# Performance work log

Hardware: AMD Instinct MI355X
Metric: run time of the kernel (lower is better)

Reference implementation:

```python
import jax, jax.numpy as jnp
import numpy as np

D = 256      # d_model
NH = 8       # num_heads
NP = 4       # n_points
H = 100      # feature map height (single level)
W = 100      # feature map width
B = 4
Q = H * W
S = H * W


def setup_inputs() -> dict:
    key = jax.random.key(0)
    ks = jax.random.split(key, 12)
    p = lambda k, shp, s=0.02: jax.random.normal(k, shp, jnp.float32) * s
    return {
        "hidden_states": jax.random.normal(ks[0], (B, Q, D), jnp.float32),
        "encoder_hidden_states": jax.random.normal(ks[1], (B, S, D), jnp.float32),
        "reference_points": jax.random.uniform(ks[2], (B, Q, 1, 2), jnp.float32),
        "spatial_shapes": jnp.array([[H, W]], dtype=jnp.int32),
        "W_off": p(ks[3], (NH * NP * 2, D)),
        "b_off": p(ks[4], (NH * NP * 2,), 0.5),
        "W_attn": p(ks[5], (NH * NP, D)),
        "b_attn": jnp.zeros((NH * NP,), jnp.float32),
        "W_val": p(ks[6], (D, D)),
        "b_val": jnp.zeros((D,), jnp.float32),
        "W_out": p(ks[7], (D, D)),
        "b_out": jnp.zeros((D,), jnp.float32),
    }


def _deform_attn(hidden_states, encoder_hidden_states, reference_points,
                 W_off, b_off, W_attn, b_attn, W_val, b_val, W_out, b_out):
    Bsz, Qn, Dm = hidden_states.shape
    d = Dm // NH

    # value projection -> [B, NH, S, d]
    value = (encoder_hidden_states @ W_val.T + b_val).reshape(Bsz, S, NH, d)
    vflat = value.transpose(0, 2, 1, 3).reshape(Bsz * NH, H * W, d)

    # sampling offsets [B,Q,NH,NP,2] (n_levels=1 squeezed)
    off = (hidden_states @ W_off.T + b_off).reshape(Bsz, Qn, NH, NP, 2)
    # attention weights softmax over (n_levels*n_points)=NP -> [B,Q,NH,NP]
    attn = jax.nn.softmax((hidden_states @ W_attn.T + b_attn).reshape(Bsz, Qn, NH, NP), axis=-1)

    # normalized sampling locations: ref + off / [W, H]
    normalizer = jnp.array([W, H], jnp.float32)
    # reference_points: [B,Q,1,2] (level dim) -> broadcast over heads/points
    loc = reference_points[:, :, None, 0, None, :] + off / normalizer  # [B,Q,NH,NP,2]

    # grid_sample semantics: grid = 2*loc - 1, align_corners=False, zeros padding
    gx = 2.0 * loc[..., 0] - 1.0
    gy = 2.0 * loc[..., 1] - 1.0
    x = ((gx + 1.0) * W - 1.0) * 0.5   # pixel coords [B,Q,NH,NP]
    y = ((gy + 1.0) * H - 1.0) * 0.5
    x0 = jnp.floor(x); y0 = jnp.floor(y)
    x1 = x0 + 1.0;     y1 = y0 + 1.0
    wx1 = x - x0; wx0 = 1.0 - wx1
    wy1 = y - y0; wy0 = 1.0 - wy1

    bh = jnp.arange(Bsz * NH)[:, None]

    def corner(xi, yi, wgt):
        valid = (xi >= 0) & (xi <= W - 1) & (yi >= 0) & (yi <= H - 1)
        xi_c = jnp.clip(xi, 0, W - 1).astype(jnp.int32)
        yi_c = jnp.clip(yi, 0, H - 1).astype(jnp.int32)
        idx = (yi_c * W + xi_c).transpose(0, 2, 1, 3).reshape(Bsz * NH, Qn * NP)
        g = vflat[bh, idx]  # [B*NH, Q*NP, d]
        wv = (wgt * valid.astype(wgt.dtype)).transpose(0, 2, 1, 3).reshape(Bsz * NH, Qn * NP, 1)
        return g * wv

    sampled = corner(x0, y0, wx0 * wy0)
    sampled = sampled + corner(x1, y0, wx1 * wy0)
    sampled = sampled + corner(x0, y1, wx0 * wy1)
    sampled = sampled + corner(x1, y1, wx1 * wy1)
    sampled = sampled.reshape(Bsz, NH, Qn, NP, d)

    out = jnp.einsum("bhqpd,bqhp->bqhd", sampled, attn).reshape(Bsz, Qn, Dm)
    return out @ W_out.T + b_out


def reference(hidden_states, encoder_hidden_states, reference_points, spatial_shapes,
              W_off, b_off, W_attn, b_attn, W_val, b_val, W_out, b_out):
    # spatial_shapes is static metadata (must equal [[H, W]]); shapes are baked in.
    return _deform_attn(hidden_states, encoder_hidden_states, reference_points,
                        W_off, b_off, W_attn, b_attn, W_val, b_val, W_out, b_out)
```

## Files before the change

### kernel.cpp

```cpp
#include <hip/hip_runtime.h>

constexpr int HH = 100;
constexpr int WW = 100;
constexpr int NH = 8;
constexpr int NP = 4;
constexpr int B  = 4;
constexpr int Q  = HH * WW;
constexpr int S  = Q;
constexpr int K  = 256;
constexpr int DH = 32;
constexpr int M  = B * Q;
constexpr int NTILES = M / 32;

typedef __attribute__((ext_vector_type(8))) short short8;
typedef __attribute__((ext_vector_type(4))) float f32x4;

struct __align__(8) ushort4_t { unsigned short x, y, z, w; };

__device__ inline unsigned short f2bf(float f) {
    unsigned u = __builtin_bit_cast(unsigned, f);
    u += 0x7fffu + ((u >> 16) & 1u);
    return (unsigned short)(u >> 16);
}
__device__ inline float bf2f(unsigned short h) {
    return __builtin_bit_cast(float, ((unsigned)h) << 16);
}
__device__ inline unsigned short f2h(float f) {
    _Float16 h = (_Float16)f;
    return __builtin_bit_cast(unsigned short, h);
}
__device__ inline float h2f(unsigned short u) {
    return (float)__builtin_bit_cast(_Float16, u);
}

__device__ inline void lds_st16s(short* base, int row, int stride, int kcol, short8 v) {
    *reinterpret_cast<short8*>(&base[row * stride + (kcol ^ ((row & 7) << 3))]) = v;
}
__device__ inline short8 lds_ld16s(const short* base, int row, int stride, int kcol) {
    return *reinterpret_cast<const short8*>(&base[row * stride + (kcol ^ ((row & 7) << 3))]);
}

__device__ inline short8 cvt8(float4 a, float4 b) {
    short8 r;
    r[0] = (short)f2bf(a.x); r[1] = (short)f2bf(a.y);
    r[2] = (short)f2bf(a.z); r[3] = (short)f2bf(a.w);
    r[4] = (short)f2bf(b.x); r[5] = (short)f2bf(b.y);
    r[6] = (short)f2bf(b.z); r[7] = (short)f2bf(b.w);
    return r;
}

__global__ __launch_bounds__(256) void preconv(
    const float* __restrict__ wval, const float* __restrict__ woff,
    const float* __restrict__ wattn, const float* __restrict__ wo,
    unsigned short* __restrict__ wbf)
{
    const int i4 = (blockIdx.x * 256 + threadIdx.x) * 4;
    const float* src;
    if (i4 < 65536) {
        src = wval + i4;
    } else if (i4 < 90112) {
        const int local = i4 - 65536;
        src = (local < 16384) ? woff + local : wattn + (local - 16384);
    } else {
        src = wo + (i4 - 90112);
    }
    const float4 f = *reinterpret_cast<const float4*>(src);
    ushort4_t o;
    o.x = f2bf(f.x); o.y = f2bf(f.y); o.z = f2bf(f.z); o.w = f2bf(f.w);
    *reinterpret_cast<ushort4_t*>(&wbf[i4]) = o;
}

__global__ __launch_bounds__(1024) void value_persist(
    const float* __restrict__ enc, const unsigned short* __restrict__ wbf,
    const float* __restrict__ bias, unsigned short* __restrict__ vflat)
{
    __shared__ short Bs[256 * 256];
    __shared__ short As[32 * 256];

    const int tid  = threadIdx.x;
    const int lane = tid & 63, w = tid >> 6;
    const int l15  = lane & 15, l4 = lane >> 4;

    const int arow = tid >> 5, ak = (tid & 31) * 8;

    int t = blockIdx.x;
    float4 fa0, fa1;
    auto lda = [&](int tt) {
        const float* s = &enc[(size_t)(tt * 32 + arow) * K + ak];
        fa0 = *reinterpret_cast<const float4*>(s);
        fa1 = *reinterpret_cast<const float4*>(s + 4);
    };
    lda(t);

    {
        const int brow = tid >> 2, kb = (tid & 3) * 64;
#pragma unroll
        for (int c = 0; c < 8; ++c) {
            short8 v = *reinterpret_cast<const short8*>(&wbf[brow * 256 + kb + c * 8]);
            lds_st16s(Bs, brow, 256, kb + c * 8, v);
        }
    }

    const int nb = w * 16;
    const int n = nb + l15;
    const float bv = bias[n];
    const int h = n >> 5, dd = n & 31;

    for (; t < NTILES; t += 256) {
        lds_st16s(As, arow, 256, ak, cvt8(fa0, fa1));
        __syncthreads();
        if (t + 256 < NTILES) lda(t + 256);

        f32x4 acc0 = {0.f, 0.f, 0.f, 0.f}, acc1 = {0.f, 0.f, 0.f, 0.f};
#pragma unroll
        for (int ks = 0; ks < 8; ++ks) {
            const int kc = ks * 32 + l4 * 8;
            const short8 bb = lds_ld16s(Bs, n, 256, kc);
            const short8 a0 = lds_ld16s(As, l15, 256, kc);
            const short8 a1 = lds_ld16s(As, 16 + l15, 256, kc);
            acc0 = __builtin_amdgcn_mfma_f32_16x16x32_bf16(a0, bb, acc0, 0, 0, 0);
            acc1 = __builtin_amdgcn_mfma_f32_16x16x32_bf16(a1, bb, acc1, 0, 0, 0);
        }
        const int m0 = t * 32;
#pragma unroll
        for (int r = 0; r < 4; ++r) {
            int m = m0 + l4 * 4 + r;
            int b_ = m / S, s_ = m - b_ * S;
            vflat[(((size_t)(b_ * NH + h)) * S + s_) * DH + dd] = f2bf(acc0[r] + bv);
            m += 16; b_ = m / S; s_ = m - b_ * S;
            vflat[(((size_t)(b_ * NH + h)) * S + s_) * DH + dd] = f2bf(acc1[r] + bv);
        }
        __syncthreads();
    }
}

__global__ __launch_bounds__(1024) void proj_persist(
    const float* __restrict__ hidden, const unsigned short* __restrict__ wbf,
    const float* __restrict__ boff, const float* __restrict__ battn,
    unsigned short* __restrict__ proj)
{
    __shared__ short Bs[96 * 256];
    __shared__ short As[32 * 256];

    const int tid  = threadIdx.x;
    const int lane = tid & 63, w = tid >> 6;
    const int l15  = lane & 15, l4 = lane >> 4;

    const int arow = tid >> 5, ak = (tid & 31) * 8;

    int t = blockIdx.x;
    float4 fa0, fa1;
    auto lda = [&](int tt) {
        const float* s = &hidden[(size_t)(tt * 32 + arow) * K + ak];
        fa0 = *reinterpret_cast<const float4*>(s);
        fa1 = *reinterpret_cast<const float4*>(s + 4);
    };
    lda(t);

    {
#pragma unroll
        for (int j = 0; j < 3; ++j) {
            const int ch = tid * 3 + j;
            const int brow = ch >> 5, kc = (ch & 31) * 8;
            short8 v = *reinterpret_cast<const short8*>(&wbf[brow * 256 + kc]);
            lds_st16s(Bs, brow, 256, kc, v);
        }
    }

    const int nf = w >> 1, mh = w & 1;
    const int n = nf * 16 + l15;
    const float bv = (w < 12) ? ((n < 64) ? boff[n] : battn[n - 64]) : 0.f;

    for (; t < NTILES; t += 512) {
        lds_st16s(As, arow, 256, ak, cvt8(fa0, fa1));
        __syncthreads();
        if (t + 512 < NTILES) lda(t + 512);

        if (w < 12) {
            f32x4 acc = {0.f, 0.f, 0.f, 0.f};
#pragma unroll
            for (int ks = 0; ks < 8; ++ks) {
                const int kc = ks * 32 + l4 * 8;
                const short8 bb = lds_ld16s(Bs, n, 256, kc);
                const short8 a = lds_ld16s(As, mh * 16 + l15, 256, kc);
                acc = __builtin_amdgcn_mfma_f32_16x16x32_bf16(a, bb, acc, 0, 0, 0);
            }
#pragma unroll
            for (int r = 0; r < 4; ++r) {
                const int m = t * 32 + mh * 16 + l4 * 4 + r;
                proj[(size_t)m * 96 + n] = f2h(acc[r] + bv);
            }
        }
        __syncthreads();
    }
}

__global__ __launch_bounds__(256) void sample_agg(
    const unsigned short* __restrict__ vflat,
    const unsigned short* __restrict__ proj,
    const float* __restrict__ ref,
    unsigned short* __restrict__ tmp)
{
    const int nblk = gridDim.x;
    const int cpx  = nblk >> 3;
    const int swz  = (blockIdx.x & 7) * cpx + (blockIdx.x >> 3);

    const int lg   = threadIdx.x >> 2;
    const int lane = threadIdx.x & 3;
    const int d0   = lane * 8;

    const int g  = swz * 64 + lg;
    const int q  = g % Q;
    const int bh = g / Q;
    const int b  = bh >> 3;
    const int h  = bh & 7;

    const size_t bq = (size_t)b * Q + q;
    const float refx = ref[bq * 2 + 0];
    const float refy = ref[bq * 2 + 1];
    const unsigned short* pr = proj + bq * 96;

    float l[NP];
#pragma unroll
    for (int p = 0; p < NP; ++p) l[p] = h2f(pr[64 + h * 4 + p]);
    const float mx = fmaxf(fmaxf(l[0], l[1]), fmaxf(l[2], l[3]));
    float e[NP];
    float esum = 0.f;
#pragma unroll
    for (int p = 0; p < NP; ++p) { e[p] = __expf(l[p] - mx); esum += e[p]; }
    const float inv = 1.f / esum;

    const unsigned short* vbase = vflat + (size_t)bh * (S * DH);

    int   cidx[NP][4];
    float cw[NP][4];
#pragma unroll
    for (int p = 0; p < NP; ++p) {
        const float ox = h2f(pr[h * 8 + p * 2 + 0]);
        const float oy = h2f(pr[h * 8 + p * 2 + 1]);
        const float x = fmaf(refx, (float)WW, ox) - 0.5f;
        const float y = fmaf(refy, (float)HH, oy) - 0.5f;
        const float x0f = floorf(x), y0f = floorf(y);
        const float wx1 = x - x0f, wx0 = 1.f - wx1;
        const float wy1 = y - y0f, wy0 = 1.f - wy1;
        const int x0 = (int)x0f, y0 = (int)y0f;
        const bool vx0 = (x0 >= 0) && (x0 < WW);
        const bool vx1 = (x0 + 1 >= 0) && (x0 + 1 < WW);
        const bool vy0 = (y0 >= 0) && (y0 < HH);
        const bool vy1 = (y0 + 1 >= 0) && (y0 + 1 < HH);
        const int xi0 = min(max(x0, 0), WW - 1);
        const int xi1 = min(max(x0 + 1, 0), WW - 1);
        const int yi0 = min(max(y0, 0), HH - 1);
        const int yi1 = min(max(y0 + 1, 0), HH - 1);
        const float ap = e[p] * inv;
        cw[p][0] = ap * wx0 * wy0 * ((vx0 && vy0) ? 1.f : 0.f);
        cw[p][1] = ap * wx1 * wy0 * ((vx1 && vy0) ? 1.f : 0.f);
        cw[p][2] = ap * wx0 * wy1 * ((vx0 && vy1) ? 1.f : 0.f);
        cw[p][3] = ap * wx1 * wy1 * ((vx1 && vy1) ? 1.f : 0.f);
        cidx[p][0] = (yi0 * WW + xi0) * DH + d0;
        cidx[p][1] = (yi0 * WW + xi1) * DH + d0;
        cidx[p][2] = (yi1 * WW + xi0) * DH + d0;
        cidx[p][3] = (yi1 * WW + xi1) * DH + d0;
    }

    float o[8];
#pragma unroll
    for (int j = 0; j < 8; ++j) o[j] = 0.f;
#pragma unroll
    for (int p = 0; p < NP; ++p) {
#pragma unroll
        for (int c = 0; c < 4; ++c) {
            const short8 v = *reinterpret_cast<const short8*>(&vbase[cidx[p][c]]);
            const float wgt = cw[p][c];
#pragma unroll
            for (int j = 0; j < 8; ++j)
                o[j] = fmaf(wgt, bf2f((unsigned short)v[j]), o[j]);
        }
    }

    short8 ov;
#pragma unroll
    for (int j = 0; j < 8; ++j) ov[j] = (short)f2bf(o[j]);
    *reinterpret_cast<short8*>(&tmp[bq * 256 + h * 32 + d0]) = ov;
}

__global__ __launch_bounds__(1024) void out_persist(
    const unsigned short* __restrict__ tmp, const unsigned short* __restrict__ wbf,
    const float* __restrict__ bias, float* __restrict__ out)
{
    __shared__ short Bs[256 * 256];
    __shared__ short As[32 * 256];

    const int tid  = threadIdx.x;
    const int lane = tid & 63, w = tid >> 6;
    const int l15  = lane & 15, l4 = lane >> 4;

    const int arow = tid >> 5, ak = (tid & 31) * 8;

    int t = blockIdx.x;
    short8 sa;
    auto lda = [&](int tt) {
        sa = *reinterpret_cast<const short8*>(&tmp[(size_t)(tt * 32 + arow) * K + ak]);
    };
    lda(t);

    {
        const int brow = tid >> 2, kb = (tid & 3) * 64;
#pragma unroll
        for (int c = 0; c < 8; ++c) {
            short8 v = *reinterpret_cast<const short8*>(&wbf[brow * 256 + kb + c * 8]);
            lds_st16s(Bs, brow, 256, kb + c * 8, v);
        }
    }

    const int n = w * 16 + l15;
    const float bv = bias[n];

    for (; t < NTILES; t += 256) {
        lds_st16s(As, arow, 256, ak, sa);
        __syncthreads();
        if (t + 256 < NTILES) lda(t + 256);

        f32x4 acc0 = {0.f, 0.f, 0.f, 0.f}, acc1 = {0.f, 0.f, 0.f, 0.f};
#pragma unroll
        for (int ks = 0; ks < 8; ++ks) {
            const int kc = ks * 32 + l4 * 8;
            const short8 bb = lds_ld16s(Bs, n, 256, kc);
            const short8 a0 = lds_ld16s(As, l15, 256, kc);
            const short8 a1 = lds_ld16s(As, 16 + l15, 256, kc);
            acc0 = __builtin_amdgcn_mfma_f32_16x16x32_bf16(a0, bb, acc0, 0, 0, 0);
            acc1 = __builtin_amdgcn_mfma_f32_16x16x32_bf16(a1, bb, acc1, 0, 0, 0);
        }
        const int m0 = t * 32;
#pragma unroll
        for (int r = 0; r < 4; ++r) {
            const int m = m0 + l4 * 4 + r;
            out[(size_t)m * K + n] = acc0[r] + bv;
            out[(size_t)(m + 16) * K + n] = acc1[r] + bv;
        }
        __syncthreads();
    }
}

extern "C" void kernel_launch(void* const* d_in, const int* in_sizes, int n_in,
                              void* d_out, int out_size, void* d_ws, size_t ws_size,
                              hipStream_t stream)
{
    const float* hidden = (const float*)d_in[0];
    const float* enc    = (const float*)d_in[1];
    const float* refp   = (const float*)d_in[2];
    const float* W_off  = (const float*)d_in[4];
    const float* b_off  = (const float*)d_in[5];
    const float* W_attn = (const float*)d_in[6];
    const float* b_attn = (const float*)d_in[7];
    const float* W_val  = (const float*)d_in[8];
    const float* b_val  = (const float*)d_in[9];
    const float* W_out  = (const float*)d_in[10];
    const float* b_out  = (const float*)d_in[11];
    float* out = (float*)d_out;

    unsigned short* vflat = (unsigned short*)d_ws;
    unsigned short* tmp   = vflat + (size_t)10240000;
    unsigned short* proj  = tmp + (size_t)10240000;
    unsigned short* wbf   = proj + (size_t)3840000;

    preconv<<<152, 256, 0, stream>>>(W_val, W_off, W_attn, W_out, wbf);

    value_persist<<<256, 1024, 0, stream>>>(enc, wbf, b_val, vflat);

    proj_persist<<<512, 1024, 0, stream>>>(hidden, wbf + 65536, b_off, b_attn, proj);

    sample_agg<<<5000, 256, 0, stream>>>(vflat, proj, refp, tmp);

    out_persist<<<256, 1024, 0, stream>>>(tmp, wbf + 90112, b_out, out);
}
```

Before: 80.17 us.

## Fuse five kernels into two: merged projections stage and fused sampling with output GEMM

Drops the separate weight-conversion kernel and converts fp32 weights to bf16 while loading them into LDS inside each GEMM kernel. The value and offset/attention projections now run in one launch with a static block split (143 value blocks, 113 projection blocks). Sampling and aggregation are fused with the output projection, so the aggregated tile goes to LDS and never round-trips through a global temporary. This removes launches and the tmp write/read, but the fused sampling kernel runs only 256 persistent blocks of 1024 threads, so there is less parallelism to hide gather latency. The fixed block split between the two GEMMs may also be unbalanced.

New measurement: 86.04 us. 7.3% more time.

```diff
diff --git a/kernel.cpp b/kernel.cpp
--- a/kernel.cpp
+++ b/kernel.cpp
@@ -15,8 +15,6 @@
 typedef __attribute__((ext_vector_type(8))) short short8;
 typedef __attribute__((ext_vector_type(4))) float f32x4;
 
-struct __align__(8) ushort4_t { unsigned short x, y, z, w; };
-
 __device__ inline unsigned short f2bf(float f) {
     unsigned u = __builtin_bit_cast(unsigned, f);
     u += 0x7fffu + ((u >> 16) & 1u);
@@ -49,294 +47,252 @@
     return r;
 }
 
-__global__ __launch_bounds__(256) void preconv(
-    const float* __restrict__ wval, const float* __restrict__ woff,
-    const float* __restrict__ wattn, const float* __restrict__ wo,
-    unsigned short* __restrict__ wbf)
+__global__ __launch_bounds__(1024) void stage1(
+    const float* __restrict__ enc, const float* __restrict__ Wval,
+    const float* __restrict__ bval, unsigned short* __restrict__ vflat,
+    const float* __restrict__ hidden, const float* __restrict__ Woff,
+    const float* __restrict__ Wattn, const float* __restrict__ boff,
+    const float* __restrict__ battn, unsigned short* __restrict__ proj)
 {
-    const int i4 = (blockIdx.x * 256 + threadIdx.x) * 4;
-    const float* src;
-    if (i4 < 65536) {
-        src = wval + i4;
-    } else if (i4 < 90112) {
-        const int local = i4 - 65536;
-        src = (local < 16384) ? woff + local : wattn + (local - 16384);
-    } else {
-        src = wo + (i4 - 90112);
-    }
-    const float4 f = *reinterpret_cast<const float4*>(src);
-    ushort4_t o;
-    o.x = f2bf(f.x); o.y = f2bf(f.y); o.z = f2bf(f.z); o.w = f2bf(f.w);
-    *reinterpret_cast<ushort4_t*>(&wbf[i4]) = o;
-}
-
-__global__ __launch_bounds__(1024) void value_persist(
-    const float* __restrict__ enc, const unsigned short* __restrict__ wbf,
-    const float* __restrict__ bias, unsigned short* __restrict__ vflat)
-{
-    __shared__ short Bs[256 * 256];
-    __shared__ short As[32 * 256];
+    __shared__ __align__(16) short SM[73728];
+    short* Bs = SM;
+    short* As = SM + 65536;
 
     const int tid  = threadIdx.x;
     const int lane = tid & 63, w = tid >> 6;
     const int l15  = lane & 15, l4 = lane >> 4;
-
     const int arow = tid >> 5, ak = (tid & 31) * 8;
 
-    int t = blockIdx.x;
-    float4 fa0, fa1;
-    auto lda = [&](int tt) {
-        const float* s = &enc[(size_t)(tt * 32 + arow) * K + ak];
-        fa0 = *reinterpret_cast<const float4*>(s);
-        fa1 = *reinterpret_cast<const float4*>(s + 4);
-    };
-    lda(t);
-
-    {
-        const int brow = tid >> 2, kb = (tid & 3) * 64;
-#pragma unroll
-        for (int c = 0; c < 8; ++c) {
-            short8 v = *reinterpret_cast<const short8*>(&wbf[brow * 256 + kb + c * 8]);
-            lds_st16s(Bs, brow, 256, kb + c * 8, v);
+    constexpr int NV = 143, NJ = 113;
+
+    if (blockIdx.x < NV) {
+        int t = blockIdx.x;
+        float4 fa0, fa1;
+        auto lda = [&](int tt) {
+            const float* s = &enc[(size_t)(tt * 32 + arow) * K + ak];
+            fa0 = *reinterpret_cast<const float4*>(s);
+            fa1 = *reinterpret_cast<const float4*>(s + 4);
+        };
+        lda(t);
+
+        {
+            const int brow = tid >> 2, kb = (tid & 3) * 64;
+#pragma unroll
+            for (int c = 0; c < 8; ++c) {
+                const float* s = &Wval[(size_t)brow * 256 + kb + c * 8];
+                float4 f0 = *reinterpret_cast<const float4*>(s);
+                float4 f1 = *reinterpret_cast<const float4*>(s + 4);
+                lds_st16s(Bs, brow, 256, kb + c * 8, cvt8(f0, f1));
+            }
+        }
+
+        const int n = w * 16 + l15;
+        const float bv = bval[n];
+        const int h = n >> 5, dd = n & 31;
+
+        for (; t < NTILES; t += NV) {
+            lds_st16s(As, arow, 256, ak, cvt8(fa0, fa1));
+            __syncthreads();
+            if (t + NV < NTILES) lda(t + NV);
+
+            f32x4 acc0 = {0.f, 0.f, 0.f, 0.f}, acc1 = {0.f, 0.f, 0.f, 0.f};
+#pragma unroll
+            for (int ks = 0; ks < 8; ++ks) {
+                const int kc = ks * 32 + l4 * 8;
+                const short8 bb = lds_ld16s(Bs, n, 256, kc);
+                const short8 a0 = lds_ld16s(As, l15, 256, kc);
+                const short8 a1 = lds_ld16s(As, 16 + l15, 256, kc);
+                acc0 = __builtin_amdgcn_mfma_f32_16x16x32_bf16(a0, bb, acc0, 0, 0, 0);
+                acc1 = __builtin_amdgcn_mfma_f32_16x16x32_bf16(a1, bb, acc1, 0, 0, 0);
+            }
+            const int m0 = t * 32;
+#pragma unroll
+            for (int r = 0; r < 4; ++r) {
+                int m = m0 + l4 * 4 + r;
+                int b_ = m / S, s_ = m - b_ * S;
+                vflat[(((size_t)(b_ * NH + h)) * S + s_) * DH + dd] = f2bf(acc0[r] + bv);
+                m += 16; b_ = m / S; s_ = m - b_ * S;
+                vflat[(((size_t)(b_ * NH + h)) * S + s_) * DH + dd] = f2bf(acc1[r] + bv);
+            }
+            __syncthreads();
+        }
+    } else {
+        int t = blockIdx.x - NV;
+        float4 fa0, fa1;
+        auto lda = [&](int tt) {
+            const float* s = &hidden[(size_t)(tt * 32 + arow) * K + ak];
+            fa0 = *reinterpret_cast<const float4*>(s);
+            fa1 = *reinterpret_cast<const float4*>(s + 4);
+        };
+        lda(t);
+
+        {
+#pragma unroll
+            for (int j = 0; j < 3; ++j) {
+                const int ch = tid * 3 + j;
+                const int brow = ch >> 5, kc = (ch & 31) * 8;
+                const float* s = (brow < 64)
+                    ? &Woff[(size_t)brow * 256 + kc]
+                    : &Wattn[(size_t)(brow - 64) * 256 + kc];
+                float4 f0 = *reinterpret_cast<const float4*>(s);
+                float4 f1 = *reinterpret_cast<const float4*>(s + 4);
+                lds_st16s(Bs, brow, 256, kc, cvt8(f0, f1));
+            }
+        }
+
+        const int nf = w >> 1, mh = w & 1;
+        const int n = nf * 16 + l15;
+        const float bv = (w < 12) ? ((n < 64) ? boff[n] : battn[n - 64]) : 0.f;
+
+        for (; t < NTILES; t += NJ) {
+            lds_st16s(As, arow, 256, ak, cvt8(fa0, fa1));
+            __syncthreads();
+            if (t + NJ < NTILES) lda(t + NJ);
+
+            if (w < 12) {
+                f32x4 acc = {0.f, 0.f, 0.f, 0.f};
+#pragma unroll
+                for (int ks = 0; ks < 8; ++ks) {
+                    const int kc = ks * 32 + l4 * 8;
+                    const short8 bb = lds_ld16s(Bs, n, 256, kc);
+                    const short8 a = lds_ld16s(As, mh * 16 + l15, 256, kc);
+                    acc = __builtin_amdgcn_mfma_f32_16x16x32_bf16(a, bb, acc, 0, 0, 0);
+                }
+#pragma unroll
+                for (int r = 0; r < 4; ++r) {
+                    const int m = t * 32 + mh * 16 + l4 * 4 + r;
+                    proj[(size_t)m * 96 + n] = f2h(acc[r] + bv);
+                }
+            }
+            __syncthreads();
         }
     }
-
-    const int nb = w * 16;
-    const int n = nb + l15;
-    const float bv = bias[n];
-    const int h = n >> 5, dd = n & 31;
-
-    for (; t < NTILES; t += 256) {
-        lds_st16s(As, arow, 256, ak, cvt8(fa0, fa1));
-        __syncthreads();
-        if (t + 256 < NTILES) lda(t + 256);
-
-        f32x4 acc0 = {0.f, 0.f, 0.f, 0.f}, acc1 = {0.f, 0.f, 0.f, 0.f};
-#pragma unroll
-        for (int ks = 0; ks < 8; ++ks) {
-            const int kc = ks * 32 + l4 * 8;
-            const short8 bb = lds_ld16s(Bs, n, 256, kc);
-            const short8 a0 = lds_ld16s(As, l15, 256, kc);
-            const short8 a1 = lds_ld16s(As, 16 + l15, 256, kc);
-            acc0 = __builtin_amdgcn_mfma_f32_16x16x32_bf16(a0, bb, acc0, 0, 0, 0);
-            acc1 = __builtin_amdgcn_mfma_f32_16x16x32_bf16(a1, bb, acc1, 0, 0, 0);
-        }
-        const int m0 = t * 32;
-#pragma unroll
-        for (int r = 0; r < 4; ++r) {
-            int m = m0 + l4 * 4 + r;
-            int b_ = m / S, s_ = m - b_ * S;
-            vflat[(((size_t)(b_ * NH + h)) * S + s_) * DH + dd] = f2bf(acc0[r] + bv);
-            m += 16; b_ = m / S; s_ = m - b_ * S;
-            vflat[(((size_t)(b_ * NH + h)) * S + s_) * DH + dd] = f2bf(acc1[r] + bv);
-        }
-        __syncthreads();
-    }
-}
-
-__global__ __launch_bounds__(1024) void proj_persist(
-    const float* __restrict__ hidden, const unsigned short* __restrict__ wbf,
-    const float* __restrict__ boff, const float* __restrict__ battn,
-    unsigned short* __restrict__ proj)
+}
+
+__global__ __launch_bounds__(1024) void sample_out(
+    const unsigned short* __restrict__ vflat,
+    const unsigned short* __restrict__ proj,
+    const float* __restrict__ ref,
+    const float* __restrict__ Wout, const float* __restrict__ bout,
+    float* __restrict__ out)
 {
-    __shared__ short Bs[96 * 256];
-    __shared__ short As[32 * 256];
+    __shared__ __align__(16) short SM[73728];
+    short* Ws = SM;
+    short* Tp = SM + 65536;
 
     const int tid  = threadIdx.x;
     const int lane = tid & 63, w = tid >> 6;
     const int l15  = lane & 15, l4 = lane >> 4;
 
-    const int arow = tid >> 5, ak = (tid & 31) * 8;
-
-    int t = blockIdx.x;
-    float4 fa0, fa1;
-    auto lda = [&](int tt) {
-        const float* s = &hidden[(size_t)(tt * 32 + arow) * K + ak];
-        fa0 = *reinterpret_cast<const float4*>(s);
-        fa1 = *reinterpret_cast<const float4*>(s + 4);
-    };
-    lda(t);
-
     {
-#pragma unroll
-        for (int j = 0; j < 3; ++j) {
-            const int ch = tid * 3 + j;
-            const int brow = ch >> 5, kc = (ch & 31) * 8;
-            short8 v = *reinterpret_cast<const short8*>(&wbf[brow * 256 + kc]);
-            lds_st16s(Bs, brow, 256, kc, v);
+        const int brow = tid >> 2, kb = (tid & 3) * 64;
+#pragma unroll
+        for (int c = 0; c < 8; ++c) {
+            const float* s = &Wout[(size_t)brow * 256 + kb + c * 8];
+            float4 f0 = *reinterpret_cast<const float4*>(s);
+            float4 f1 = *reinterpret_cast<const float4*>(s + 4);
+            lds_st16s(Ws, brow, 256, kb + c * 8, cvt8(f0, f1));
         }
     }
 
-    const int nf = w >> 1, mh = w & 1;
-    const int n = nf * 16 + l15;
-    const float bv = (w < 12) ? ((n < 64) ? boff[n] : battn[n - 64]) : 0.f;
-
-    for (; t < NTILES; t += 512) {
-        lds_st16s(As, arow, 256, ak, cvt8(fa0, fa1));
+    const int n = w * 16 + l15;
+    const float bv = bout[n];
+
+    const int r   = tid >> 5;
+    const int rem = tid & 31;
+    const int h   = rem >> 2;
+    const int d0  = (rem & 3) * 8;
+
+    for (int t = blockIdx.x; t < NTILES; t += 256) {
+        {
+            const int m = t * 32 + r;
+            const int b = m / Q;
+            const unsigned short* pr = proj + (size_t)m * 96;
+            const float refx = ref[(size_t)m * 2 + 0];
+            const float refy = ref[(size_t)m * 2 + 1];
+
+            float l[NP];
+#pragma unroll
+            for (int p = 0; p < NP; ++p) l[p] = h2f(pr[64 + h * 4 + p]);
+            const float mx = fmaxf(fmaxf(l[0], l[1]), fmaxf(l[2], l[3]));
+            float e[NP]; float esum = 0.f;
+#pragma unroll
+            for (int p = 0; p < NP; ++p) { e[p] = __expf(l[p] - mx); esum += e[p]; }
+            const float inv = 1.f / esum;
+
+            const unsigned short* vbase = vflat + (size_t)(b * NH + h) * (S * DH);
+
+            int   cidx[NP][4];
+            float cw[NP][4];
+#pragma unroll
+            for (int p = 0; p < NP; ++p) {
+                const float ox = h2f(pr[h * 8 + p * 2 + 0]);
+                const float oy = h2f(pr[h * 8 + p * 2 + 1]);
+                const float x = fmaf(refx, (float)WW, ox) - 0.5f;
+                const float y = fmaf(refy, (float)HH, oy) - 0.5f;
+                const float x0f = floorf(x), y0f = floorf(y);
+                const float wx1 = x - x0f, wx0 = 1.f - wx1;
+                const float wy1 = y - y0f, wy0 = 1.f - wy1;
+                const int x0 = (int)x0f, y0 = (int)y0f;
+                const bool vx0 = (x0 >= 0) && (x0 < WW);
+                const bool vx1 = (x0 + 1 >= 0) && (x0 + 1 < WW);
+                const bool vy0 = (y0 >= 0) && (y0 < HH);
+                const bool vy1 = (y0 + 1 >= 0) && (y0 + 1 < HH);
+                const int xi0 = min(max(x0, 0), WW - 1);
+                const int xi1 = min(max(x0 + 1, 0), WW - 1);
+                const int yi0 = min(max(y0, 0), HH - 1);
+                const int yi1 = min(max(y0 + 1, 0), HH - 1);
+                const float ap = e[p] * inv;
+                cw[p][0] = ap * wx0 * wy0 * ((vx0 && vy0) ? 1.f : 0.f);
+                cw[p][1] = ap * wx1 * wy0 * ((vx1 && vy0) ? 1.f : 0.f);
+                cw[p][2] = ap * wx0 * wy1 * ((vx0 && vy1) ? 1.f : 0.f);
+                cw[p][3] = ap * wx1 * wy1 * ((vx1 && vy1) ? 1.f : 0.f);
+                cidx[p][0] = (yi0 * WW + xi0) * DH + d0;
+                cidx[p][1] = (yi0 * WW + xi1) * DH + d0;
+                cidx[p][2] = (yi1 * WW + xi0) * DH + d0;
+                cidx[p][3] = (yi1 * WW + xi1) * DH + d0;
+            }
+
+            float o[8];
+#pragma unroll
+            for (int j = 0; j < 8; ++j) o[j] = 0.f;
+#pragma unroll
+            for (int p = 0; p < NP; ++p) {
+#pragma unroll
+                for (int c = 0; c < 4; ++c) {
+                    const short8 v = *reinterpret_cast<const short8*>(&vbase[cidx[p][c]]);
+                    const float wgt = cw[p][c];
+#pragma unroll
+                    for (int j = 0; j < 8; ++j)
+                        o[j] = fmaf(wgt, bf2f((unsigned short)v[j]), o[j]);
+                }
+            }
+
+            short8 ov;
+#pragma unroll
+            for (int j = 0; j < 8; ++j) ov[j] = (short)f2bf(o[j]);
+            lds_st16s(Tp, r, 256, h * 32 + d0, ov);
+        }
         __syncthreads();
-        if (t + 512 < NTILES) lda(t + 512);
-
-        if (w < 12) {
-            f32x4 acc = {0.f, 0.f, 0.f, 0.f};
+
+        {
+            f32x4 acc0 = {0.f, 0.f, 0.f, 0.f}, acc1 = {0.f, 0.f, 0.f, 0.f};
 #pragma unroll
             for (int ks = 0; ks < 8; ++ks) {
                 const int kc = ks * 32 + l4 * 8;
-                const short8 bb = lds_ld16s(Bs, n, 256, kc);
-                const short8 a = lds_ld16s(As, mh * 16 + l15, 256, kc);
-                acc = __builtin_amdgcn_mfma_f32_16x16x32_bf16(a, bb, acc, 0, 0, 0);
-            }
-#pragma unroll
-            for (int r = 0; r < 4; ++r) {
-                const int m = t * 32 + mh * 16 + l4 * 4 + r;
-                proj[(size_t)m * 96 + n] = f2h(acc[r] + bv);
-            }
-        }
-        __syncthreads();
-    }
-}
-
-__global__ __launch_bounds__(256) void sample_agg(
-    const unsigned short* __restrict__ vflat,
-    const unsigned short* __restrict__ proj,
-    const float* __restrict__ ref,
-    unsigned short* __restrict__ tmp)
-{
-    const int nblk = gridDim.x;
-    const int cpx  = nblk >> 3;
-    const int swz  = (blockIdx.x & 7) * cpx + (blockIdx.x >> 3);
-
-    const int lg   = threadIdx.x >> 2;
-    const int lane = threadIdx.x & 3;
-    const int d0   = lane * 8;
-
-    const int g  = swz * 64 + lg;
-    const int q  = g % Q;
-    const int bh = g / Q;
-    const int b  = bh >> 3;
-    const int h  = bh & 7;
-
-    const size_t bq = (size_t)b * Q + q;
-    const float refx = ref[bq * 2 + 0];
-    const float refy = ref[bq * 2 + 1];
-    const unsigned short* pr = proj + bq * 96;
-
-    float l[NP];
-#pragma unroll
-    for (int p = 0; p < NP; ++p) l[p] = h2f(pr[64 + h * 4 + p]);
-    const float mx = fmaxf(fmaxf(l[0], l[1]), fmaxf(l[2], l[3]));
-    float e[NP];
-    float esum = 0.f;
-#pragma unroll
-    for (int p = 0; p < NP; ++p) { e[p] = __expf(l[p] - mx); esum += e[p]; }
-    const float inv = 1.f / esum;
-
-    const unsigned short* vbase = vflat + (size_t)bh * (S * DH);
-
-    int   cidx[NP][4];
-    float cw[NP][4];
-#pragma unroll
-    for (int p = 0; p < NP; ++p) {
-        const float ox = h2f(pr[h * 8 + p * 2 + 0]);
-        const float oy = h2f(pr[h * 8 + p * 2 + 1]);
-        const float x = fmaf(refx, (float)WW, ox) - 0.5f;
-        const float y = fmaf(refy, (float)HH, oy) - 0.5f;
-        const float x0f = floorf(x), y0f = floorf(y);
-        const float wx1 = x - x0f, wx0 = 1.f - wx1;
-        const float wy1 = y - y0f, wy0 = 1.f - wy1;
-        const int x0 = (int)x0f, y0 = (int)y0f;
-        const bool vx0 = (x0 >= 0) && (x0 < WW);
-        const bool vx1 = (x0 + 1 >= 0) && (x0 + 1 < WW);
-        const bool vy0 = (y0 >= 0) && (y0 < HH);
-        const bool vy1 = (y0 + 1 >= 0) && (y0 + 1 < HH);
-        const int xi0 = min(max(x0, 0), WW - 1);
-        const int xi1 = min(max(x0 + 1, 0), WW - 1);
-        const int yi0 = min(max(y0, 0), HH - 1);
-        const int yi1 = min(max(y0 + 1, 0), HH - 1);
-        const float ap = e[p] * inv;
-        cw[p][0] = ap * wx0 * wy0 * ((vx0 && vy0) ? 1.f : 0.f);
-        cw[p][1] = ap * wx1 * wy0 * ((vx1 && vy0) ? 1.f : 0.f);
-        cw[p][2] = ap * wx0 * wy1 * ((vx0 && vy1) ? 1.f : 0.f);
-        cw[p][3] = ap * wx1 * wy1 * ((vx1 && vy1) ? 1.f : 0.f);
-        cidx[p][0] = (yi0 * WW + xi0) * DH + d0;
-        cidx[p][1] = (yi0 * WW + xi1) * DH + d0;
-        cidx[p][2] = (yi1 * WW + xi0) * DH + d0;
-        cidx[p][3] = (yi1 * WW + xi1) * DH + d0;
-    }
-
-    float o[8];
-#pragma unroll
-    for (int j = 0; j < 8; ++j) o[j] = 0.f;
-#pragma unroll
-    for (int p = 0; p < NP; ++p) {
-#pragma unroll
-        for (int c = 0; c < 4; ++c) {
-            const short8 v = *reinterpret_cast<const short8*>(&vbase[cidx[p][c]]);
-            const float wgt = cw[p][c];
-#pragma unroll
-            for (int j = 0; j < 8; ++j)
-                o[j] = fmaf(wgt, bf2f((unsigned short)v[j]), o[j]);
-        }
-    }
-
-    short8 ov;
-#pragma unroll
-    for (int j = 0; j < 8; ++j) ov[j] = (short)f2bf(o[j]);
-    *reinterpret_cast<short8*>(&tmp[bq * 256 + h * 32 + d0]) = ov;
-}
-
-__global__ __launch_bounds__(1024) void out_persist(
-    const unsigned short* __restrict__ tmp, const unsigned short* __restrict__ wbf,
-    const float* __restrict__ bias, float* __restrict__ out)
-{
-    __shared__ short Bs[256 * 256];
-    __shared__ short As[32 * 256];
-
-    const int tid  = threadIdx.x;
-    const int lane = tid & 63, w = tid >> 6;
-    const int l15  = lane & 15, l4 = lane >> 4;
-
-    const int arow = tid >> 5, ak = (tid & 31) * 8;
-
-    int t = blockIdx.x;
-    short8 sa;
-    auto lda = [&](int tt) {
-        sa = *reinterpret_cast<const short8*>(&tmp[(size_t)(tt * 32 + arow) * K + ak]);
-    };
-    lda(t);
-
-    {
-        const int brow = tid >> 2, kb = (tid & 3) * 64;
-#pragma unroll
-        for (int c = 0; c < 8; ++c) {
-            short8 v = *reinterpret_cast<const short8*>(&wbf[brow * 256 + kb + c * 8]);
-            lds_st16s(Bs, brow, 256, kb + c * 8, v);
-        }
-    }
-
-    const int n = w * 16 + l15;
-    const float bv = bias[n];
-
-    for (; t < NTILES; t += 256) {
-        lds_st16s(As, arow, 256, ak, sa);
-        __syncthreads();
-        if (t + 256 < NTILES) lda(t + 256);
-
-        f32x4 acc0 = {0.f, 0.f, 0.f, 0.f}, acc1 = {0.f, 0.f, 0.f, 0.f};
-#pragma unroll
-        for (int ks = 0; ks < 8; ++ks) {
-            const int kc = ks * 32 + l4 * 8;
-            const short8 bb = lds_ld16s(Bs, n, 256, kc);
-            const short8 a0 = lds_ld16s(As, l15, 256, kc);
-            const short8 a1 = lds_ld16s(As, 16 + l15, 256, kc);
-            acc0 = __builtin_amdgcn_mfma_f32_16x16x32_bf16(a0, bb, acc0, 0, 0, 0);
-            acc1 = __builtin_amdgcn_mfma_f32_16x16x32_bf16(a1, bb, acc1, 0, 0, 0);
-        }
-        const int m0 = t * 32;
-#pragma unroll
-        for (int r = 0; r < 4; ++r) {
-            const int m = m0 + l4 * 4 + r;
-            out[(size_t)m * K + n] = acc0[r] + bv;
-            out[(size_t)(m + 16) * K + n] = acc1[r] + bv;
+                const short8 bb = lds_ld16s(Ws, n, 256, kc);
+                const short8 a0 = lds_ld16s(Tp, l15, 256, kc);
+                const short8 a1 = lds_ld16s(Tp, 16 + l15, 256, kc);
+                acc0 = __builtin_amdgcn_mfma_f32_16x16x32_bf16(a0, bb, acc0, 0, 0, 0);
+                acc1 = __builtin_amdgcn_mfma_f32_16x16x32_bf16(a1, bb, acc1, 0, 0, 0);
+            }
+            const int m0 = t * 32;
+#pragma unroll
+            for (int r2 = 0; r2 < 4; ++r2) {
+                const int m = m0 + l4 * 4 + r2;
+                out[(size_t)m * K + n] = acc0[r2] + bv;
+                out[(size_t)(m + 16) * K + n] = acc1[r2] + bv;
+            }
         }
         __syncthreads();
     }
@@ -360,17 +316,10 @@
     float* out = (float*)d_out;
 
     unsigned short* vflat = (unsigned short*)d_ws;
-    unsigned short* tmp   = vflat + (size_t)10240000;
-    unsigned short* proj  = tmp + (size_t)10240000;
-    unsigned short* wbf   = proj + (size_t)3840000;
-
-    preconv<<<152, 256, 0, stream>>>(W_val, W_off, W_attn, W_out, wbf);
-
-    value_persist<<<256, 1024, 0, stream>>>(enc, wbf, b_val, vflat);
-
-    proj_persist<<<512, 1024, 0, stream>>>(hidden, wbf + 65536, b_off, b_attn, proj);
-
-    sample_agg<<<5000, 256, 0, stream>>>(vflat, proj, refp, tmp);
-
-    out_persist<<<256, 1024, 0, stream>>>(tmp, wbf + 90112, b_out, out);
-}
+    unsigned short* proj  = vflat + (size_t)10240000;
+
+    stage1<<<256, 1024, 0, stream>>>(
+        enc, W_val, b_val, vflat, hidden, W_off, W_attn, b_off, b_attn, proj);
+
+    sample_out<<<256, 1024, 0, stream>>>(vflat, proj, refp, W_out, b_out, out);
+}
```
